# Performance work log

Measured on AMD Instinct MI355X. Metric: run time of the kernel, lower is better.

## Reference

```python
import jax, jax.numpy as jnp
import numpy as np

N_NODES = 50000
N_EDGES = 800000
HID = 128
N_PROC = 3  # num_layers - 1 processor iterations (shared weights)


def _mlp(x, w1, b1, w2, b2, w3, b3):
    h = jax.nn.relu(x @ w1 + b1)
    h = jax.nn.relu(h @ w2 + b2)
    return h @ w3 + b3


def setup_inputs() -> dict:
    key = jax.random.key(0)
    ks = jax.random.split(key, 32)

    def p(k, shape):
        fan_in = shape[0]
        return (jax.random.normal(k, shape, dtype=jnp.float32) / np.float32(np.sqrt(fan_in)))

    inp = {
        "X_curr": jax.random.normal(ks[0], (N_NODES, 6), dtype=jnp.float32),
        "y_prev": jax.random.normal(ks[1], (N_NODES,), dtype=jnp.float32),
        "edge": jax.random.randint(ks[2], (2, N_EDGES), 0, N_NODES, dtype=jnp.int32),
        "mode": 0,
        # EdgeModel net: Linear(9,H) ReLU Linear(H,H) ReLU Linear(H,3)
        "ew1": p(ks[3], (9, HID)), "eb1": jnp.zeros((HID,), jnp.float32),
        "ew2": p(ks[4], (HID, HID)), "eb2": jnp.zeros((HID,), jnp.float32),
        "ew3": p(ks[5], (HID, 3)), "eb3": jnp.zeros((3,), jnp.float32),
        # NodeModel net: Linear(5,H) ReLU Linear(H,H) ReLU Linear(H,1)
        "nw1": p(ks[6], (5, HID)), "nb1": jnp.zeros((HID,), jnp.float32),
        "nw2": p(ks[7], (HID, HID)), "nb2": jnp.zeros((HID,), jnp.float32),
        "nw3": p(ks[8], (HID, 1)), "nb3": jnp.zeros((1,), jnp.float32),
        # decoder: Linear(5,H) ReLU Linear(H,H) ReLU Linear(H,H) ReLU Linear(H,1)
        "dw1": p(ks[9], (5, HID)), "db1": jnp.zeros((HID,), jnp.float32),
        "dw2": p(ks[10], (HID, HID)), "db2": jnp.zeros((HID,), jnp.float32),
        "dw3": p(ks[11], (HID, HID)), "db3": jnp.zeros((HID,), jnp.float32),
        "dw4": p(ks[12], (HID, 1)), "db4": jnp.zeros((1,), jnp.float32),
    }
    return inp


def reference(X_curr, y_prev,
              ew1, eb1, ew2, eb2, ew3, eb3,
              nw1, nb1, nw2, nb2, nw3, nb3,
              dw1, db1, dw2, db2, dw3, db3, dw4, db4,
              edge, mode):
    n = X_curr.shape[0]
    src_idx, dst_idx = edge[0], edge[1]
    # x_in = cat(X_curr[:, [0,1,2,4]], y_prev)  -> [N, 5]
    x = jnp.concatenate([X_curr[:, jnp.array([0, 1, 2, 4])], y_prev[:, None]], axis=-1)

    # _compute_edge_attr: grad_r = (f_dest - f_src) * disp_r
    xs, xd = x[src_idx], x[dst_idx]
    disp = xd[:, :3] - xs[:, :3]
    edge_attr = (xd[:, 4] - xs[:, 4])[:, None] * disp  # [E, 3]

    # degree for scatter-mean (nodes with no incoming edges aggregate to 0)
    deg = jax.ops.segment_sum(jnp.ones((edge.shape[1],), x.dtype), dst_idx, num_segments=n)
    inv_deg = jnp.where(deg > 0, 1.0 / jnp.maximum(deg, 1.0), 0.0)

    for _ in range(N_PROC):
        # EdgeModel
        xs, xd = x[src_idx], x[dst_idx]
        disp = xd[:, :3] - xs[:, :3]
        norm_r = jnp.linalg.norm(disp, axis=-1, keepdims=True)
        net_in = jnp.concatenate([disp, norm_r, edge_attr, xs[:, 4:5], xd[:, 4:5]], axis=-1)  # [E, 9]
        edge_attr = edge_attr + _mlp(net_in, ew1, eb1, ew2, eb2, ew3, eb3)
        # NodeModel: message = edge_attr, aggr='mean' at target (edge[1])
        aggr = jax.ops.segment_sum(edge_attr, dst_idx, num_segments=n) * inv_deg[:, None]  # [N, 3]
        node_in = jnp.concatenate([x[:, 3:5], aggr], axis=-1)  # [N, 5]
        delta = _mlp(node_in, nw1, nb1, nw2, nb2, nw3, nb3)[:, 0]
        x = x.at[:, 4].add(delta)

    # decoder
    h = jax.nn.relu(x @ dw1 + db1)
    h = jax.nn.relu(h @ dw2 + db2)
    h = jax.nn.relu(h @ dw3 + db3)
    x_out = h @ dw4 + db4  # [N, 1]
    return y_prev + x_out[:, 0]
```

## Files before the change

kernel.cpp:

```cpp
#include <hip/hip_runtime.h>

typedef float f32x4 __attribute__((ext_vector_type(4)));
typedef __bf16 bf16x8 __attribute__((ext_vector_type(8)));
typedef __bf16 bf16x4 __attribute__((ext_vector_type(4)));

#define WB_W1E 0
#define WB_W2E 4096
#define WB_W3E 20480
#define WB_W1N 22528
#define WB_W2N 26624
#define WB_W3N 43008
#define WB_W1D 45056
#define WB_W2D 49152
#define WB_W3D 65536
#define WB_W4D 81920
#define WB_TOTAL 83968

__global__ void k_prep(const float* __restrict__ ew1, const float* __restrict__ eb1,
                       const float* __restrict__ ew2, const float* __restrict__ ew3,
                       const float* __restrict__ nw1, const float* __restrict__ nb1,
                       const float* __restrict__ nw2, const float* __restrict__ nw3,
                       const float* __restrict__ dw1, const float* __restrict__ db1,
                       const float* __restrict__ dw2, const float* __restrict__ dw3,
                       const float* __restrict__ dw4, __bf16* __restrict__ wb) {
  int gid = blockIdx.x * 256 + threadIdx.x;
  if (gid >= WB_TOTAL) return;
  const float* srcs[10] = {ew1, ew2, ew3, nw1, nw2, nw3, dw1, dw2, dw3, dw4};
  const float* brow[10] = {eb1, 0, 0, nb1, 0, 0, db1, 0, 0, 0};
  const int Ks[10] = {9, 128, 128, 5, 128, 128, 5, 128, 128, 128};
  const int Ns[10] = {128, 128, 3, 128, 128, 1, 128, 128, 128, 1};
  const int CTs[10] = {8, 8, 1, 8, 8, 1, 8, 8, 8, 1};
  const int cum[11] = {0, 4096, 20480, 22528, 26624, 43008, 45056, 49152, 65536, 81920, 83968};
  int seg = 0;
  while (gid >= cum[seg + 1]) seg++;
  int li = gid - cum[seg];
  int j = li & 7;
  int lane = (li >> 3) & 63;
  int fi = li >> 9;
  int CT = CTs[seg];
  int ct = fi % CT;
  int kt = fi / CT;
  int k = kt * 32 + ((lane >> 4) << 3) + j;
  int n = ct * 16 + (lane & 15);
  int kl;
  if (seg == 0) {
    if (k < 4) kl = k;
    else if (k >= 8 && k < 13) kl = k - 4;
    else kl = (k == 13) ? -2 : -1;
  } else if (seg == 3 || seg == 6) {
    if (k < 5) kl = k;
    else kl = (k == 5) ? -2 : -1;
  } else {
    kl = (k < Ks[seg]) ? k : -1;
  }
  float v = 0.f;
  if (n < Ns[seg]) {
    if (kl >= 0) v = srcs[seg][kl * Ns[seg] + n];
    else if (kl == -2 && brow[seg]) v = brow[seg][n];
  }
  wb[gid] = (__bf16)v;
}

__global__ void k_zero(const float* __restrict__ y_prev, float* __restrict__ x4,
                       int* __restrict__ cnt, int n) {
  int i = blockIdx.x * 256 + threadIdx.x;
  if (i < n) {
    x4[i] = y_prev[i];
    cnt[i] = 0;
  }
}

__global__ void k_count(const int* __restrict__ dstp, int* __restrict__ cnt, int E) {
  int e = blockIdx.x * 256 + threadIdx.x;
  if (e < E) atomicAdd(cnt + dstp[e], 1);
}

__global__ void k_scan_block(const int* __restrict__ cnt, int* __restrict__ rp,
                             float* __restrict__ invdeg, int* __restrict__ bsum, int n) {
  __shared__ int sd[256];
  int t = threadIdx.x;
  int i = blockIdx.x * 256 + t;
  int c = (i < n) ? cnt[i] : 0;
  if (i < n) invdeg[i] = c > 0 ? 1.0f / (float)c : 0.f;
  sd[t] = c;
  __syncthreads();
#pragma unroll
  for (int off = 1; off < 256; off <<= 1) {
    int v = sd[t];
    int u = (t >= off) ? sd[t - off] : 0;
    __syncthreads();
    sd[t] = v + u;
    __syncthreads();
  }
  if (i < n) rp[i] = sd[t] - c;
  if (t == 255) bsum[blockIdx.x] = sd[255];
}

__global__ void k_scan_top(int* __restrict__ bsum, int nb) {
  __shared__ int sd[1024];
  int t = threadIdx.x;
  int c = (t < nb) ? bsum[t] : 0;
  sd[t] = c;
  __syncthreads();
#pragma unroll
  for (int off = 1; off < 1024; off <<= 1) {
    int v = sd[t];
    int u = (t >= off) ? sd[t - off] : 0;
    __syncthreads();
    sd[t] = v + u;
    __syncthreads();
  }
  if (t < nb) bsum[t] = sd[t] - c;
}

__global__ void k_scan_add(int* __restrict__ rp, const int* __restrict__ bsum, int n) {
  int i = blockIdx.x * 256 + threadIdx.x;
  if (i < n) rp[i] += bsum[blockIdx.x];
}

__global__ void k_scatter(const float* __restrict__ Xc, const float* __restrict__ y_prev,
                          const int* __restrict__ src, const int* __restrict__ dstp,
                          int* __restrict__ rp, int* __restrict__ srcS, int* __restrict__ dstS,
                          float* __restrict__ peS, float* __restrict__ eaS, int E) {
  int e = blockIdx.x * 256 + threadIdx.x;
  if (e >= E) return;
  int s = src[e], d = dstp[e];
  float dx = Xc[d * 6 + 0] - Xc[s * 6 + 0];
  float dy = Xc[d * 6 + 1] - Xc[s * 6 + 1];
  float dz = Xc[d * 6 + 2] - Xc[s * 6 + 2];
  float nr = sqrtf(dx * dx + dy * dy + dz * dz);
  float w = y_prev[d] - y_prev[s];
  int p = atomicAdd(rp + d, 1);
  srcS[p] = s;
  dstS[p] = d;
  f32x4 pv = {dx, dy, dz, nr};
  *(f32x4*)(peS + 4 * p) = pv;
  f32x4 av = {w * dx, w * dy, w * dz, 0.f};
  *(f32x4*)(eaS + 4 * p) = av;
}

__global__ void k_gather(const float* __restrict__ eaS, const int* __restrict__ rp,
                         const float* __restrict__ invdeg, float* __restrict__ aggr, int n) {
  int i = blockIdx.x * 256 + threadIdx.x;
  if (i >= n) return;
  int s = (i == 0) ? 0 : rp[i - 1];
  int e = rp[i];
  f32x4 acc = {0.f, 0.f, 0.f, 0.f};
#pragma unroll 2
  for (int p = s; p < e; p++) {
    f32x4 v = *(const f32x4*)(eaS + 4 * p);
    acc[0] += v[0];
    acc[1] += v[1];
    acc[2] += v[2];
  }
  float iv = invdeg[i];
  f32x4 o = {acc[0] * iv, acc[1] * iv, acc[2] * iv, 0.f};
  *(f32x4*)(aggr + 4 * i) = o;
}

__device__ __forceinline__ int aoff(int row, int b) { return (row * 256 + b) ^ ((row & 7) << 4); }

__device__ __forceinline__ void wg_sync() {
  asm volatile("s_waitcnt lgkmcnt(0)" ::: "memory");
  __builtin_amdgcn_s_barrier();
}

__device__ __forceinline__ bf16x4 relu_pack(f32x4 a) {
  bf16x4 p;
#pragma unroll
  for (int r = 0; r < 4; r++) {
    float v = a[r];
    p[r] = (__bf16)(v > 0.f ? v : 0.f);
  }
  return p;
}

__global__ __attribute__((amdgpu_flat_work_group_size(256, 256), amdgpu_waves_per_eu(3, 4))) void
k_edge(const float* __restrict__ x4, const float* __restrict__ pe, float* __restrict__ ea,
       const int* __restrict__ src, const int* __restrict__ dstp,
       const __bf16* __restrict__ W1f, const __bf16* __restrict__ W2f,
       const __bf16* __restrict__ W3f, const float* __restrict__ b2,
       const float* __restrict__ b3, int ntiles, int E) {
  __shared__ char Ab[16384];
  __shared__ char Bb[16384];
  const int tid = threadIdx.x;
  const int l = tid & 63, w = tid >> 6;
  const int col = l & 15, krow = l >> 4;
  const int rl = w * 16 + (l >> 2), chunk = l & 3;

  bf16x8 w1r[2], w2r[4][2], w3r[4];
#pragma unroll
  for (int t = 0; t < 2; t++) w1r[t] = *(const bf16x8*)(W1f + ((2 * w + t) << 9) + l * 8);
#pragma unroll
  for (int kt = 0; kt < 4; kt++)
#pragma unroll
    for (int t = 0; t < 2; t++)
      w2r[kt][t] = *(const bf16x8*)(W2f + ((kt * 8 + 2 * w + t) << 9) + l * 8);
#pragma unroll
  for (int kt = 0; kt < 4; kt++) w3r[kt] = *(const bf16x8*)(W3f + (kt << 9) + l * 8);
  f32x4 b2c[2];
#pragma unroll
  for (int t = 0; t < 2; t++) b2c[t] = *(const f32x4*)(b2 + (2 * w + t) * 16 + krow * 4);
  f32x4 b3i = {0.f, 0.f, 0.f, 0.f};
  if (krow == 0) {
    b3i[0] = b3[0];
    b3i[1] = b3[1];
    b3i[2] = b3[2];
  }

  int tile = blockIdx.x;
  if (tile >= ntiles) return;

  int e0 = tile * 64 + rl;
  int ec = e0 < E ? e0 : E - 1;
  int cs = src[ec], cd = dstp[ec];
  f32x4 cld = {0.f, 0.f, 0.f, 0.f};
  if (chunk < 2) cld = *(const f32x4*)(((chunk == 1) ? ea : pe) + 4 * ec);
  float cxs = 0.f, cxd = 0.f;
  if (chunk == 1) {
    cxs = x4[cs];
    cxd = x4[cd];
  }

  for (;;) {
    bf16x8 v;
#pragma unroll
    for (int q = 0; q < 8; q++) v[q] = (__bf16)0.f;
    if (chunk == 0) {
      v[0] = (__bf16)cld[0];
      v[1] = (__bf16)cld[1];
      v[2] = (__bf16)cld[2];
      v[3] = (__bf16)cld[3];
    } else if (chunk == 1) {
      v[0] = (__bf16)cld[0];
      v[1] = (__bf16)cld[1];
      v[2] = (__bf16)cld[2];
      v[3] = (__bf16)cxs;
      v[4] = (__bf16)cxd;
      v[5] = (__bf16)1.0f;
    }
    *(bf16x8*)(Ab + aoff(rl, chunk * 16)) = v;

    int nt = tile + (int)gridDim.x;
    bool hn = nt < ntiles;
    int tc = hn ? nt : tile;
    int en = tc * 64 + rl;
    if (en >= E) en = E - 1;
    int ns = src[en], nd = dstp[en];

    wg_sync();

    f32x4 h[4][2];
#pragma unroll
    for (int c = 0; c < 4; c++)
#pragma unroll
      for (int t = 0; t < 2; t++) {
        f32x4 z = {0.f, 0.f, 0.f, 0.f};
        h[c][t] = z;
      }
    bf16x8 bb[4];
#pragma unroll
    for (int c = 0; c < 4; c++) bb[c] = *(const bf16x8*)(Ab + aoff(c * 16 + col, krow * 16));
#pragma unroll
    for (int c = 0; c < 4; c++)
#pragma unroll
      for (int t = 0; t < 2; t++)
        h[c][t] = __builtin_amdgcn_mfma_f32_16x16x32_bf16(w1r[t], bb[c], h[c][t], 0, 0, 0);
#pragma unroll
    for (int c = 0; c < 4; c++)
#pragma unroll
      for (int t = 0; t < 2; t++)
        *(bf16x4*)(Bb + aoff(c * 16 + col, (2 * w + t) * 32 + krow * 8)) = relu_pack(h[c][t]);

    wg_sync();

    f32x4 nld = {0.f, 0.f, 0.f, 0.f};
    if (chunk < 2) nld = *(const f32x4*)(((chunk == 1) ? ea : pe) + 4 * en);
    float nxs = 0.f, nxd = 0.f;
    if (chunk == 1) {
      nxs = x4[ns];
      nxd = x4[nd];
    }

#pragma unroll
    for (int c = 0; c < 4; c++)
#pragma unroll
      for (int t = 0; t < 2; t++) h[c][t] = b2c[t];
#pragma unroll
    for (int kt = 0; kt < 4; kt++) {
#pragma unroll
      for (int c = 0; c < 4; c++)
        bb[c] = *(const bf16x8*)(Bb + aoff(c * 16 + col, kt * 64 + krow * 16));
#pragma unroll
      for (int c = 0; c < 4; c++)
#pragma unroll
        for (int t = 0; t < 2; t++)
          h[c][t] = __builtin_amdgcn_mfma_f32_16x16x32_bf16(w2r[kt][t], bb[c], h[c][t], 0, 0, 0);
    }
#pragma unroll
    for (int c = 0; c < 4; c++)
#pragma unroll
      for (int t = 0; t < 2; t++)
        *(bf16x4*)(Ab + aoff(c * 16 + col, (2 * w + t) * 32 + krow * 8)) = relu_pack(h[c][t]);

    wg_sync();

    f32x4 o = b3i;
#pragma unroll
    for (int kt = 0; kt < 4; kt++) {
      bf16x8 bq = *(const bf16x8*)(Ab + aoff(w * 16 + col, kt * 64 + krow * 16));
      o = __builtin_amdgcn_mfma_f32_16x16x32_bf16(w3r[kt], bq, o, 0, 0, 0);
    }

    if (krow == 0) {
      int e3 = tile * 64 + w * 16 + col;
      if (e3 < E) {
        f32x4 oe = *(const f32x4*)(ea + 4 * e3);
        f32x4 nv;
        nv[0] = oe[0] + o[0];
        nv[1] = oe[1] + o[1];
        nv[2] = oe[2] + o[2];
        nv[3] = 0.f;
        *(f32x4*)(ea + 4 * e3) = nv;
      }
    }

    if (!hn) break;
    tile = nt;
    cld = nld;
    cxs = nxs;
    cxd = nxd;
  }
}

__global__ __attribute__((amdgpu_flat_work_group_size(256, 256), amdgpu_waves_per_eu(3, 4))) void
k_node(float* __restrict__ x4, const float* __restrict__ Xc, const float* __restrict__ aggr,
       const __bf16* __restrict__ W1f, const __bf16* __restrict__ W2f,
       const __bf16* __restrict__ W3f, const float* __restrict__ b2,
       const float* __restrict__ b3, int n) {
  __shared__ char Ab[16384];
  __shared__ char Bb[16384];
  const int tid = threadIdx.x;
  const int l = tid & 63, w = tid >> 6;
  const int col = l & 15, krow = l >> 4;
  const int rl = w * 16 + (l >> 2), chunk = l & 3;

  bf16x8 w1r[2], w2r[4][2], w3r[4];
#pragma unroll
  for (int t = 0; t < 2; t++) w1r[t] = *(const bf16x8*)(W1f + ((2 * w + t) << 9) + l * 8);
#pragma unroll
  for (int kt = 0; kt < 4; kt++)
#pragma unroll
    for (int t = 0; t < 2; t++)
      w2r[kt][t] = *(const bf16x8*)(W2f + ((kt * 8 + 2 * w + t) << 9) + l * 8);
#pragma unroll
  for (int kt = 0; kt < 4; kt++) w3r[kt] = *(const bf16x8*)(W3f + (kt << 9) + l * 8);
  f32x4 b2c[2];
#pragma unroll
  for (int t = 0; t < 2; t++) b2c[t] = *(const f32x4*)(b2 + (2 * w + t) * 16 + krow * 4);
  float b3s = b3[0];

  int tile = blockIdx.x;
  int i0 = tile * 64 + rl;
  bool vi = i0 < n;
  int i = vi ? i0 : (n - 1);

  bf16x8 v;
#pragma unroll
  for (int q = 0; q < 8; q++) v[q] = (__bf16)0.f;
  if (chunk == 0) {
    float x3 = Xc[i * 6 + 4];
    float xv = x4[i];
    f32x4 ag = *(const f32x4*)(aggr + 4 * i);
    v[0] = (__bf16)x3;
    v[1] = (__bf16)xv;
    v[2] = (__bf16)ag[0];
    v[3] = (__bf16)ag[1];
    v[4] = (__bf16)ag[2];
    v[5] = (__bf16)1.0f;
  }
  *(bf16x8*)(Ab + aoff(rl, chunk * 16)) = v;

  wg_sync();

  f32x4 h[4][2];
#pragma unroll
  for (int c = 0; c < 4; c++)
#pragma unroll
    for (int t = 0; t < 2; t++) {
      f32x4 z = {0.f, 0.f, 0.f, 0.f};
      h[c][t] = z;
    }
  bf16x8 bb[4];
#pragma unroll
  for (int c = 0; c < 4; c++) bb[c] = *(const bf16x8*)(Ab + aoff(c * 16 + col, krow * 16));
#pragma unroll
  for (int c = 0; c < 4; c++)
#pragma unroll
    for (int t = 0; t < 2; t++)
      h[c][t] = __builtin_amdgcn_mfma_f32_16x16x32_bf16(w1r[t], bb[c], h[c][t], 0, 0, 0);
#pragma unroll
  for (int c = 0; c < 4; c++)
#pragma unroll
    for (int t = 0; t < 2; t++)
      *(bf16x4*)(Bb + aoff(c * 16 + col, (2 * w + t) * 32 + krow * 8)) = relu_pack(h[c][t]);

  wg_sync();

#pragma unroll
  for (int c = 0; c < 4; c++)
#pragma unroll
    for (int t = 0; t < 2; t++) h[c][t] = b2c[t];
#pragma unroll
  for (int kt = 0; kt < 4; kt++) {
#pragma unroll
    for (int c = 0; c < 4; c++)
      bb[c] = *(const bf16x8*)(Bb + aoff(c * 16 + col, kt * 64 + krow * 16));
#pragma unroll
    for (int c = 0; c < 4; c++)
#pragma unroll
      for (int t = 0; t < 2; t++)
        h[c][t] = __builtin_amdgcn_mfma_f32_16x16x32_bf16(w2r[kt][t], bb[c], h[c][t], 0, 0, 0);
  }
#pragma unroll
  for (int c = 0; c < 4; c++)
#pragma unroll
    for (int t = 0; t < 2; t++)
      *(bf16x4*)(Ab + aoff(c * 16 + col, (2 * w + t) * 32 + krow * 8)) = relu_pack(h[c][t]);

  wg_sync();

  f32x4 o = {0.f, 0.f, 0.f, 0.f};
  if (krow == 0) o[0] = b3s;
#pragma unroll
  for (int kt = 0; kt < 4; kt++) {
    bf16x8 bq = *(const bf16x8*)(Ab + aoff(w * 16 + col, kt * 64 + krow * 16));
    o = __builtin_amdgcn_mfma_f32_16x16x32_bf16(w3r[kt], bq, o, 0, 0, 0);
  }

  if (krow == 0) {
    int i3 = tile * 64 + w * 16 + col;
    if (i3 < n) x4[i3] = x4[i3] + o[0];
  }
}

__global__ __attribute__((amdgpu_flat_work_group_size(256, 256), amdgpu_waves_per_eu(2, 4))) void
k_dec(const float* __restrict__ x4, const float* __restrict__ Xc, const float* __restrict__ y_prev,
      const __bf16* __restrict__ W1f, const __bf16* __restrict__ W2f,
      const __bf16* __restrict__ W3f, const __bf16* __restrict__ W4f,
      const float* __restrict__ b2, const float* __restrict__ b3, const float* __restrict__ b4,
      float* __restrict__ out, int n) {
  __shared__ char Ab[16384];
  __shared__ char Bb[16384];
  const int tid = threadIdx.x;
  const int l = tid & 63, w = tid >> 6;
  const int col = l & 15, krow = l >> 4;
  const int rl = w * 16 + (l >> 2), chunk = l & 3;

  bf16x8 w1r[2], w2r[4][2], w3r[4][2], w4r[4];
#pragma unroll
  for (int t = 0; t < 2; t++) w1r[t] = *(const bf16x8*)(W1f + ((2 * w + t) << 9) + l * 8);
#pragma unroll
  for (int kt = 0; kt < 4; kt++)
#pragma unroll
    for (int t = 0; t < 2; t++) {
      w2r[kt][t] = *(const bf16x8*)(W2f + ((kt * 8 + 2 * w + t) << 9) + l * 8);
      w3r[kt][t] = *(const bf16x8*)(W3f + ((kt * 8 + 2 * w + t) << 9) + l * 8);
    }
#pragma unroll
  for (int kt = 0; kt < 4; kt++) w4r[kt] = *(const bf16x8*)(W4f + (kt << 9) + l * 8);
  f32x4 b2c[2], b3c[2];
#pragma unroll
  for (int t = 0; t < 2; t++) {
    b2c[t] = *(const f32x4*)(b2 + (2 * w + t) * 16 + krow * 4);
    b3c[t] = *(const f32x4*)(b3 + (2 * w + t) * 16 + krow * 4);
  }
  float b4s = b4[0];

  int tile = blockIdx.x;
  int i0 = tile * 64 + rl;
  bool vi = i0 < n;
  int i = vi ? i0 : (n - 1);

  bf16x8 v;
#pragma unroll
  for (int q = 0; q < 8; q++) v[q] = (__bf16)0.f;
  if (chunk == 0) {
    v[0] = (__bf16)Xc[i * 6 + 0];
    v[1] = (__bf16)Xc[i * 6 + 1];
    v[2] = (__bf16)Xc[i * 6 + 2];
    v[3] = (__bf16)Xc[i * 6 + 4];
    v[4] = (__bf16)x4[i];
    v[5] = (__bf16)1.0f;
  }
  *(bf16x8*)(Ab + aoff(rl, chunk * 16)) = v;

  wg_sync();

  f32x4 h[4][2];
  bf16x8 bb[4];
#pragma unroll
  for (int c = 0; c < 4; c++)
#pragma unroll
    for (int t = 0; t < 2; t++) {
      f32x4 z = {0.f, 0.f, 0.f, 0.f};
      h[c][t] = z;
    }
#pragma unroll
  for (int c = 0; c < 4; c++) bb[c] = *(const bf16x8*)(Ab + aoff(c * 16 + col, krow * 16));
#pragma unroll
  for (int c = 0; c < 4; c++)
#pragma unroll
    for (int t = 0; t < 2; t++)
      h[c][t] = __builtin_amdgcn_mfma_f32_16x16x32_bf16(w1r[t], bb[c], h[c][t], 0, 0, 0);
#pragma unroll
  for (int c = 0; c < 4; c++)
#pragma unroll
    for (int t = 0; t < 2; t++)
      *(bf16x4*)(Bb + aoff(c * 16 + col, (2 * w + t) * 32 + krow * 8)) = relu_pack(h[c][t]);

  wg_sync();

#pragma unroll
  for (int c = 0; c < 4; c++)
#pragma unroll
    for (int t = 0; t < 2; t++) h[c][t] = b2c[t];
#pragma unroll
  for (int kt = 0; kt < 4; kt++) {
#pragma unroll
    for (int c = 0; c < 4; c++)
      bb[c] = *(const bf16x8*)(Bb + aoff(c * 16 + col, kt * 64 + krow * 16));
#pragma unroll
    for (int c = 0; c < 4; c++)
#pragma unroll
      for (int t = 0; t < 2; t++)
        h[c][t] = __builtin_amdgcn_mfma_f32_16x16x32_bf16(w2r[kt][t], bb[c], h[c][t], 0, 0, 0);
  }
#pragma unroll
  for (int c = 0; c < 4; c++)
#pragma unroll
    for (int t = 0; t < 2; t++)
      *(bf16x4*)(Ab + aoff(c * 16 + col, (2 * w + t) * 32 + krow * 8)) = relu_pack(h[c][t]);

  wg_sync();

#pragma unroll
  for (int c = 0; c < 4; c++)
#pragma unroll
    for (int t = 0; t < 2; t++) h[c][t] = b3c[t];
#pragma unroll
  for (int kt = 0; kt < 4; kt++) {
#pragma unroll
    for (int c = 0; c < 4; c++)
      bb[c] = *(const bf16x8*)(Ab + aoff(c * 16 + col, kt * 64 + krow * 16));
#pragma unroll
    for (int c = 0; c < 4; c++)
#pragma unroll
      for (int t = 0; t < 2; t++)
        h[c][t] = __builtin_amdgcn_mfma_f32_16x16x32_bf16(w3r[kt][t], bb[c], h[c][t], 0, 0, 0);
  }
#pragma unroll
  for (int c = 0; c < 4; c++)
#pragma unroll
    for (int t = 0; t < 2; t++)
      *(bf16x4*)(Bb + aoff(c * 16 + col, (2 * w + t) * 32 + krow * 8)) = relu_pack(h[c][t]);

  wg_sync();

  f32x4 o = {0.f, 0.f, 0.f, 0.f};
  if (krow == 0) o[0] = b4s;
#pragma unroll
  for (int kt = 0; kt < 4; kt++) {
    bf16x8 bq = *(const bf16x8*)(Bb + aoff(w * 16 + col, kt * 64 + krow * 16));
    o = __builtin_amdgcn_mfma_f32_16x16x32_bf16(w4r[kt], bq, o, 0, 0, 0);
  }

  if (krow == 0) {
    int i3 = tile * 64 + w * 16 + col;
    if (i3 < n) out[i3] = y_prev[i3] + o[0];
  }
}

extern "C" void kernel_launch(void* const* d_in, const int* in_sizes, int n_in, void* d_out,
                              int out_size, void* d_ws, size_t ws_size, hipStream_t stream) {
  const float* Xc = (const float*)d_in[0];
  const float* y_prev = (const float*)d_in[1];
  const int* edge = (const int*)d_in[2];
  const float* ew1 = (const float*)d_in[4];
  const float* eb1 = (const float*)d_in[5];
  const float* ew2 = (const float*)d_in[6];
  const float* eb2 = (const float*)d_in[7];
  const float* ew3 = (const float*)d_in[8];
  const float* eb3 = (const float*)d_in[9];
  const float* nw1 = (const float*)d_in[10];
  const float* nb1 = (const float*)d_in[11];
  const float* nw2 = (const float*)d_in[12];
  const float* nb2 = (const float*)d_in[13];
  const float* nw3 = (const float*)d_in[14];
  const float* nb3 = (const float*)d_in[15];
  const float* dw1 = (const float*)d_in[16];
  const float* db1 = (const float*)d_in[17];
  const float* dw2 = (const float*)d_in[18];
  const float* db2 = (const float*)d_in[19];
  const float* dw3 = (const float*)d_in[20];
  const float* db3 = (const float*)d_in[21];
  const float* dw4 = (const float*)d_in[22];
  const float* db4 = (const float*)d_in[23];

  int n = in_sizes[0] / 6;
  int E = in_sizes[2] / 2;
  const int* srcp = edge;
  const int* dstp = edge + E;

  __bf16* wb = (__bf16*)d_ws;
  float* fbase = (float*)((char*)d_ws + (size_t)WB_TOTAL * 2);
  size_t na = ((size_t)n + 3) & ~(size_t)3;
  float* x4 = fbase;
  float* invdeg = fbase + na;
  float* aggr = fbase + 2 * na;
  int* cnt = (int*)(fbase + 6 * na);
  int* rp = cnt + na;
  int* bsum = rp + na + 8;
  int* srcS = bsum + 1024;
  int* dstS = srcS + E;
  float* peS = (float*)(dstS + E);
  float* eaS = peS + 4 * (size_t)E;

  size_t need = (size_t)WB_TOTAL * 2 + (8 * na + 8 + 1024 + 10 * (size_t)E) * 4;
  if (ws_size < need) return;

  dim3 B(256);
  int nblk = (n + 255) / 256;
  k_prep<<<dim3((WB_TOTAL + 255) / 256), B, 0, stream>>>(ew1, eb1, ew2, ew3, nw1, nb1, nw2, nw3,
                                                         dw1, db1, dw2, dw3, dw4, wb);
  k_zero<<<dim3(nblk), B, 0, stream>>>(y_prev, x4, cnt, n);
  k_count<<<dim3((E + 255) / 256), B, 0, stream>>>(dstp, cnt, E);
  k_scan_block<<<dim3(nblk), B, 0, stream>>>(cnt, rp, invdeg, bsum, n);
  k_scan_top<<<dim3(1), dim3(1024), 0, stream>>>(bsum, nblk);
  k_scan_add<<<dim3(nblk), B, 0, stream>>>(rp, bsum, n);
  k_scatter<<<dim3((E + 255) / 256), B, 0, stream>>>(Xc, y_prev, srcp, dstp, rp, srcS, dstS, peS,
                                                     eaS, E);

  int etiles = (E + 63) / 64;
  int vtiles = (n + 63) / 64;
  int egrid = etiles < 768 ? etiles : 768;
  for (int it = 0; it < 3; it++) {
    k_edge<<<dim3(egrid), B, 0, stream>>>(x4, peS, eaS, srcS, dstS, wb + WB_W1E, wb + WB_W2E,
                                          wb + WB_W3E, eb2, eb3, etiles, E);
    k_gather<<<dim3((n + 255) / 256), B, 0, stream>>>(eaS, rp, invdeg, aggr, n);
    k_node<<<dim3(vtiles), B, 0, stream>>>(x4, Xc, aggr, wb + WB_W1N, wb + WB_W2N, wb + WB_W3N,
                                           nb2, nb3, n);
  }
  k_dec<<<dim3(vtiles), B, 0, stream>>>(x4, Xc, y_prev, wb + WB_W1D, wb + WB_W2D, wb + WB_W3D,
                                        wb + WB_W4D, db2, db3, db4, (float*)d_out, n);
}
```

Before: 294.7 us.

## Build dst-sorted edge arrays via bucketed LDS binning instead of global atomics

Replaces the per-edge global atomicAdd scatter that builds the dst-sorted CSR edge arrays with a two-pass bucketed scheme. First, edges are binned into buckets of 64 destination nodes using LDS histograms and one global atomic per bucket per block. Then one block per bucket computes the edge features and places each edge using LDS atomics. The row pointer stays an exclusive scan with rp[n]=E, and the gather reads rp[i]..rp[i+1]. The aim is to cut global atomic contention and scattered writes during preprocessing; the risk is that a bucket holding more than 4096 edges would silently drop edges.

Measured after the change: 303.1 us. 2.9% more time.

```diff
diff --git a/kernel.cpp b/kernel.cpp
--- a/kernel.cpp
+++ b/kernel.cpp
@@ -15,6 +15,9 @@
 #define WB_W3D 65536
 #define WB_W4D 81920
 #define WB_TOTAL 83968
+
+#define BKT_SHIFT 6
+#define BKT_SZ 64
 
 __global__ void k_prep(const float* __restrict__ ew1, const float* __restrict__ eb1,
                        const float* __restrict__ ew2, const float* __restrict__ ew3,
@@ -113,38 +116,108 @@
   if (t < nb) bsum[t] = sd[t] - c;
 }
 
-__global__ void k_scan_add(int* __restrict__ rp, const int* __restrict__ bsum, int n) {
+__global__ void k_scan_add(int* __restrict__ rp, const int* __restrict__ bsum, int n, int E) {
   int i = blockIdx.x * 256 + threadIdx.x;
   if (i < n) rp[i] += bsum[blockIdx.x];
-}
-
-__global__ void k_scatter(const float* __restrict__ Xc, const float* __restrict__ y_prev,
-                          const int* __restrict__ src, const int* __restrict__ dstp,
-                          int* __restrict__ rp, int* __restrict__ srcS, int* __restrict__ dstS,
-                          float* __restrict__ peS, float* __restrict__ eaS, int E) {
-  int e = blockIdx.x * 256 + threadIdx.x;
-  if (e >= E) return;
-  int s = src[e], d = dstp[e];
-  float dx = Xc[d * 6 + 0] - Xc[s * 6 + 0];
-  float dy = Xc[d * 6 + 1] - Xc[s * 6 + 1];
-  float dz = Xc[d * 6 + 2] - Xc[s * 6 + 2];
-  float nr = sqrtf(dx * dx + dy * dy + dz * dz);
-  float w = y_prev[d] - y_prev[s];
-  int p = atomicAdd(rp + d, 1);
-  srcS[p] = s;
-  dstS[p] = d;
-  f32x4 pv = {dx, dy, dz, nr};
-  *(f32x4*)(peS + 4 * p) = pv;
-  f32x4 av = {w * dx, w * dy, w * dz, 0.f};
-  *(f32x4*)(eaS + 4 * p) = av;
+  if (i == 0) rp[n] = E;
+}
+
+__global__ void k_initcur(const int* __restrict__ rp, int* __restrict__ cur, int nbkt, int n) {
+  int b = blockIdx.x * 256 + threadIdx.x;
+  if (b < nbkt) {
+    int d = b << BKT_SHIFT;
+    if (d > n) d = n;
+    cur[b] = rp[d];
+  }
+}
+
+__global__ __launch_bounds__(256) void k_bin(const int* __restrict__ dstp, int* __restrict__ cur,
+                                             int* __restrict__ eix, int nbkt, int E) {
+  __shared__ int hist[1024];
+  __shared__ int base[1024];
+  int tid = threadIdx.x;
+  for (int t = tid; t < nbkt; t += 256) hist[t] = 0;
+  __syncthreads();
+  int e0 = blockIdx.x * 8192;
+  int b[32], lr[32];
+#pragma unroll
+  for (int j = 0; j < 32; j++) {
+    int e = e0 + j * 256 + tid;
+    if (e < E) {
+      b[j] = dstp[e] >> BKT_SHIFT;
+      lr[j] = atomicAdd(&hist[b[j]], 1);
+    } else {
+      b[j] = -1;
+      lr[j] = 0;
+    }
+  }
+  __syncthreads();
+  for (int t = tid; t < nbkt; t += 256) {
+    int c = hist[t];
+    base[t] = c ? atomicAdd(&cur[t], c) : 0;
+  }
+  __syncthreads();
+#pragma unroll
+  for (int j = 0; j < 32; j++)
+    if (b[j] >= 0) eix[base[b[j]] + lr[j]] = e0 + j * 256 + tid;
+}
+
+__global__ __launch_bounds__(256) void k_build(const int* __restrict__ srcO,
+                                               const int* __restrict__ dstO,
+                                               const float* __restrict__ Xc,
+                                               const float* __restrict__ yp,
+                                               const int* __restrict__ rp, const int* eix,
+                                               int* __restrict__ srcS, int* dstS,
+                                               float* __restrict__ peS, float* __restrict__ eaS,
+                                               int n) {
+  __shared__ int rpl[BKT_SZ + 1];
+  __shared__ int cnt[BKT_SZ];
+  int tid = threadIdx.x;
+  int d0 = blockIdx.x << BKT_SHIFT;
+  if (tid <= BKT_SZ) {
+    int d = d0 + tid;
+    if (d > n) d = n;
+    rpl[tid] = rp[d];
+  }
+  if (tid < BKT_SZ) cnt[tid] = 0;
+  __syncthreads();
+  int dlim = n - d0;
+  if (dlim > BKT_SZ) dlim = BKT_SZ;
+  int gstart = rpl[0], gend = rpl[dlim];
+  int ei[16];
+#pragma unroll
+  for (int k = 0; k < 16; k++) {
+    int p = gstart + k * 256 + tid;
+    ei[k] = (p < gend) ? eix[p] : -1;
+  }
+  __syncthreads();
+#pragma unroll
+  for (int k = 0; k < 16; k++) {
+    int e = ei[k];
+    if (e < 0) continue;
+    int s = srcO[e], d = dstO[e];
+    float dx = Xc[d * 6 + 0] - Xc[s * 6 + 0];
+    float dy = Xc[d * 6 + 1] - Xc[s * 6 + 1];
+    float dz = Xc[d * 6 + 2] - Xc[s * 6 + 2];
+    float nr = sqrtf(dx * dx + dy * dy + dz * dz);
+    float w = yp[d] - yp[s];
+    int r = atomicAdd(&cnt[d - d0], 1);
+    int q = rpl[d - d0] + r;
+    srcS[q] = s;
+    dstS[q] = d;
+    f32x4 pv = {dx, dy, dz, nr};
+    *(f32x4*)(peS + 4 * q) = pv;
+    f32x4 av = {w * dx, w * dy, w * dz, 0.f};
+    *(f32x4*)(eaS + 4 * q) = av;
+  }
 }
 
 __global__ void k_gather(const float* __restrict__ eaS, const int* __restrict__ rp,
                          const float* __restrict__ invdeg, float* __restrict__ aggr, int n) {
   int i = blockIdx.x * 256 + threadIdx.x;
   if (i >= n) return;
-  int s = (i == 0) ? 0 : rp[i - 1];
-  int e = rp[i];
+  int s = rp[i];
+  int e = rp[i + 1];
   f32x4 acc = {0.f, 0.f, 0.f, 0.f};
 #pragma unroll 2
   for (int p = s; p < e; p++) {
@@ -631,15 +704,17 @@
 
   dim3 B(256);
   int nblk = (n + 255) / 256;
+  int nbkt = (n + BKT_SZ - 1) / BKT_SZ;
   k_prep<<<dim3((WB_TOTAL + 255) / 256), B, 0, stream>>>(ew1, eb1, ew2, ew3, nw1, nb1, nw2, nw3,
                                                          dw1, db1, dw2, dw3, dw4, wb);
   k_zero<<<dim3(nblk), B, 0, stream>>>(y_prev, x4, cnt, n);
   k_count<<<dim3((E + 255) / 256), B, 0, stream>>>(dstp, cnt, E);
   k_scan_block<<<dim3(nblk), B, 0, stream>>>(cnt, rp, invdeg, bsum, n);
   k_scan_top<<<dim3(1), dim3(1024), 0, stream>>>(bsum, nblk);
-  k_scan_add<<<dim3(nblk), B, 0, stream>>>(rp, bsum, n);
-  k_scatter<<<dim3((E + 255) / 256), B, 0, stream>>>(Xc, y_prev, srcp, dstp, rp, srcS, dstS, peS,
-                                                     eaS, E);
+  k_scan_add<<<dim3(nblk), B, 0, stream>>>(rp, bsum, n, E);
+  k_initcur<<<dim3((nbkt + 255) / 256), B, 0, stream>>>(rp, bsum, nbkt, n);
+  k_bin<<<dim3((E + 8191) / 8192), B, 0, stream>>>(dstp, bsum, dstS, nbkt, E);
+  k_build<<<dim3(nbkt), B, 0, stream>>>(srcp, dstp, Xc, y_prev, rp, dstS, srcS, dstS, peS, eaS, n);
 
   int etiles = (E + 63) / 64;
   int vtiles = (n + 63) / 64;
```
